# Performance work log

Measured on AMD Instinct MI355X. Metric: run time of the kernel, lower is better.

The kernel has to match this reference:

```python
import jax, jax.numpy as jnp
import numpy as np

EPS = 1e-6
N_HEADS = 16
N_KV_HEADS = 4
HEAD_DIM = 128
DIM = 2048
SEQ = 2048
BATCH = 2


def _make_freqs_cis(seqlen, head_dim, theta=10000.0):
    inv = 1.0 / (theta ** (jnp.arange(0, head_dim, 2, dtype=jnp.float32) / head_dim))  # [hd/2]
    t = jnp.arange(seqlen, dtype=jnp.float32)
    ang = jnp.outer(t, inv)  # [seq, hd/2]
    return jnp.stack([jnp.cos(ang), jnp.sin(ang)], axis=-1)  # [seq, hd/2, 2]


def setup_inputs() -> dict:
    key = jax.random.key(0)
    k1, k2, k3 = jax.random.split(key, 3)
    std = 0.02
    x = jax.random.normal(k1, (BATCH, SEQ, DIM), dtype=jnp.float32)
    freqs_cis = _make_freqs_cis(SEQ, HEAD_DIM)
    norm_w = jnp.ones((DIM,), dtype=jnp.float32)
    wqkv_w = jax.random.normal(k2, ((N_HEADS + 2 * N_KV_HEADS) * HEAD_DIM, DIM), dtype=jnp.float32) * std
    wo_w = jax.random.normal(k3, (DIM, N_HEADS * HEAD_DIM), dtype=jnp.float32) * std
    return {"x": x, "freqs_cis": freqs_cis, "norm_w": norm_w, "wqkv_w": wqkv_w, "wo_w": wo_w}


def _rope(t, cos, sin):
    # t: [b, s, h, hd] viewed as pairs; cos/sin: [s, hd/2]
    b, s, h, hd = t.shape
    tr = t.reshape(b, s, h, hd // 2, 2)
    xr, xi = tr[..., 0], tr[..., 1]
    c = cos[None, :, None, :]
    sn = sin[None, :, None, :]
    out_r = xr * c - xi * sn
    out_i = xr * sn + xi * c
    return jnp.stack([out_r, out_i], axis=-1).reshape(b, s, h, hd)


def reference(x, freqs_cis, norm_w, wqkv_w, wo_w):
    bs, seqlen, dim = x.shape
    n_rep = N_HEADS // N_KV_HEADS
    # RMSNorm
    xn = x * jax.lax.rsqrt(jnp.mean(x * x, axis=-1, keepdims=True) + EPS) * norm_w
    # fused QKV projection
    qkv = jnp.einsum('bsd,ed->bse', xn, wqkv_w)
    q_sz = N_HEADS * HEAD_DIM
    kv_sz = N_KV_HEADS * HEAD_DIM
    xq = qkv[..., :q_sz].reshape(bs, seqlen, N_HEADS, HEAD_DIM)
    xk = qkv[..., q_sz:q_sz + kv_sz].reshape(bs, seqlen, N_KV_HEADS, HEAD_DIM)
    xv = qkv[..., q_sz + kv_sz:].reshape(bs, seqlen, N_KV_HEADS, HEAD_DIM)
    cos, sin = freqs_cis[..., 0], freqs_cis[..., 1]
    xq = _rope(xq, cos, sin)
    xk = _rope(xk, cos, sin)
    # GQA: group q heads so kv broadcast replaces repeat_kv materialization
    q = xq.transpose(0, 2, 1, 3).reshape(bs, N_KV_HEADS, n_rep, seqlen, HEAD_DIM)
    k = xk.transpose(0, 2, 1, 3)  # [b, g, s, d]
    v = xv.transpose(0, 2, 1, 3)
    scale = 1.0 / jnp.sqrt(jnp.float32(HEAD_DIM))
    scores = jnp.einsum('bgrqd,bgkd->bgrqk', q, k) * scale
    causal = jnp.tril(jnp.ones((seqlen, seqlen), dtype=bool))
    scores = jnp.where(causal, scores, jnp.finfo(scores.dtype).min)
    probs = jax.nn.softmax(scores, axis=-1)
    out = jnp.einsum('bgrqk,bgkd->bgrqd', probs, v)
    out = out.reshape(bs, N_HEADS, seqlen, HEAD_DIM).transpose(0, 2, 1, 3).reshape(bs, seqlen, N_HEADS * HEAD_DIM)
    return jnp.einsum('bse,de->bsd', out, wo_w)
```

## Files before the change

### kernel.cpp

```cpp
#include <hip/hip_runtime.h>
#include <cstdint>
#include <cstddef>

typedef __bf16 bhalf;
typedef __bf16 bhalf8 __attribute__((ext_vector_type(8)));
typedef __bf16 bhalf4 __attribute__((ext_vector_type(4)));
typedef float f32x4 __attribute__((ext_vector_type(4)));

#define RMS_EPS 1e-6f
#define N_HEADS 16
#define N_KV 4
#define HD 128
#define DIM 2048
#define SEQ 2048
#define BATCH 2

static __device__ __forceinline__ f32x4 mfma16(bhalf8 a, bhalf8 b, f32x4 c) {
    return __builtin_amdgcn_mfma_f32_16x16x32_bf16(a, b, c, 0, 0, 0);
}

static __device__ __forceinline__ void gload16(const bhalf* g, bhalf* l) {
    __builtin_amdgcn_global_load_lds((const __attribute__((address_space(1))) unsigned int*)g,
                                     (__attribute__((address_space(3))) unsigned int*)l,
                                     16, 0, 0);
}

__global__ __launch_bounds__(256) void cvt_w(const float* __restrict__ a,
                                             const float* __restrict__ b,
                                             bhalf* __restrict__ dst) {
    size_t i = ((size_t)blockIdx.x * 256 + threadIdx.x) * 4;
    const size_t NQ = (size_t)3072 * 2048;
    float4 v = (i < NQ) ? ((const float4*)a)[i >> 2] : ((const float4*)b)[(i - NQ) >> 2];
    bhalf4 o;
    o[0] = (bhalf)v.x; o[1] = (bhalf)v.y; o[2] = (bhalf)v.z; o[3] = (bhalf)v.w;
    *(bhalf4*)(dst + i) = o;
}

__global__ __launch_bounds__(256) void rmsnorm_k(const float* __restrict__ x,
                                                 const float* __restrict__ w,
                                                 bhalf* __restrict__ xn) {
    const int row = blockIdx.x;
    const int tid = threadIdx.x;
    const float4* xr = (const float4*)(x + (size_t)row * DIM);
    float4 v0 = xr[tid * 2], v1 = xr[tid * 2 + 1];
    float ss = v0.x * v0.x + v0.y * v0.y + v0.z * v0.z + v0.w * v0.w
             + v1.x * v1.x + v1.y * v1.y + v1.z * v1.z + v1.w * v1.w;
    #pragma unroll
    for (int off = 32; off; off >>= 1) ss += __shfl_xor(ss, off, 64);
    __shared__ float red[4];
    if ((tid & 63) == 0) red[tid >> 6] = ss;
    __syncthreads();
    float tot = red[0] + red[1] + red[2] + red[3];
    float scale = rsqrtf(tot * (1.0f / DIM) + RMS_EPS);
    const float4* wr = (const float4*)w;
    float4 w0 = wr[tid * 2], w1 = wr[tid * 2 + 1];
    bhalf8 o;
    o[0] = (bhalf)(v0.x * scale * w0.x); o[1] = (bhalf)(v0.y * scale * w0.y);
    o[2] = (bhalf)(v0.z * scale * w0.z); o[3] = (bhalf)(v0.w * scale * w0.w);
    o[4] = (bhalf)(v1.x * scale * w1.x); o[5] = (bhalf)(v1.y * scale * w1.y);
    o[6] = (bhalf)(v1.z * scale * w1.z); o[7] = (bhalf)(v1.w * scale * w1.w);
    *(bhalf8*)(xn + (size_t)row * DIM + tid * 8) = o;
}

__global__ __launch_bounds__(256) void gemm_abt(const bhalf* __restrict__ A,
                                                const bhalf* __restrict__ B,
                                                float* __restrict__ C,
                                                int N, int K) {
    const int tid = threadIdx.x;
    const int wave = tid >> 6, lane = tid & 63;
    const int quad = lane >> 4, r16 = lane & 15;
    const int m0 = blockIdx.y * 128, n0 = blockIdx.x * 128;
    const int wm = (wave >> 1) * 64, wn = (wave & 1) * 64;

    __shared__ __align__(16) bhalf sA[128][32];
    __shared__ __align__(16) bhalf sB[128][32];

    f32x4 acc[4][4];
    #pragma unroll
    for (int i = 0; i < 4; ++i)
        #pragma unroll
        for (int j = 0; j < 4; ++j) acc[i][j] = (f32x4)0.0f;

    const int lrow = lane >> 2;
    const int lcol = (lane & 3) * 8;
    const int arow = 32 * wave + lrow;
    const bhalf* Ap = A + (size_t)(m0 + arow) * K + lcol;
    const bhalf* Bp = B + (size_t)(n0 + arow) * K + lcol;
    const size_t rs16 = (size_t)16 * K;
    bhalf* sAp0 = &sA[32 * wave][0];
    bhalf* sAp1 = &sA[32 * wave + 16][0];
    bhalf* sBp0 = &sB[32 * wave][0];
    bhalf* sBp1 = &sB[32 * wave + 16][0];

    for (int k0 = 0; k0 < K; k0 += 32) {
        __syncthreads();
        gload16(Ap + k0, sAp0);
        gload16(Ap + k0 + rs16, sAp1);
        gload16(Bp + k0, sBp0);
        gload16(Bp + k0 + rs16, sBp1);
        __syncthreads();
        bhalf8 af[4], bfr[4];
        #pragma unroll
        for (int i = 0; i < 4; ++i) af[i]  = *(bhalf8*)&sA[wm + i * 16 + r16][quad * 8];
        #pragma unroll
        for (int j = 0; j < 4; ++j) bfr[j] = *(bhalf8*)&sB[wn + j * 16 + r16][quad * 8];
        #pragma unroll
        for (int i = 0; i < 4; ++i)
            #pragma unroll
            for (int j = 0; j < 4; ++j)
                acc[i][j] = mfma16(af[i], bfr[j], acc[i][j]);
    }

    #pragma unroll
    for (int i = 0; i < 4; ++i) {
        const int rbase = m0 + wm + i * 16 + quad * 4;
        #pragma unroll
        for (int rr = 0; rr < 4; ++rr) {
            float* crow = C + (size_t)(rbase + rr) * N + n0 + wn + r16;
            #pragma unroll
            for (int j = 0; j < 4; ++j) crow[j * 16] = acc[i][j][rr];
        }
    }
}

__global__ __launch_bounds__(256) void rope_k(const float* __restrict__ qkv,
                                              const float* __restrict__ freqs,
                                              bhalf* __restrict__ qb,
                                              bhalf* __restrict__ kb,
                                              bhalf* __restrict__ vt) {
    const int bs = blockIdx.x;
    const int b = bs >> 11, s = bs & 2047;
    const float* row = qkv + (size_t)bs * 3072;
    const int tid = threadIdx.x;

    {
        const int h = tid >> 4, d20 = (tid & 15) * 4;
        const float* rp = row + h * HD + d20 * 2;
        float4 e0 = *(const float4*)rp;
        float4 e1 = *(const float4*)(rp + 4);
        const float* fp = freqs + (size_t)s * 128 + d20 * 2;
        float4 f0 = *(const float4*)fp;
        float4 f1 = *(const float4*)(fp + 4);
        bhalf8 o;
        o[0] = (bhalf)(e0.x * f0.x - e0.y * f0.y); o[1] = (bhalf)(e0.x * f0.y + e0.y * f0.x);
        o[2] = (bhalf)(e0.z * f0.z - e0.w * f0.w); o[3] = (bhalf)(e0.z * f0.w + e0.w * f0.z);
        o[4] = (bhalf)(e1.x * f1.x - e1.y * f1.y); o[5] = (bhalf)(e1.x * f1.y + e1.y * f1.x);
        o[6] = (bhalf)(e1.z * f1.z - e1.w * f1.w); o[7] = (bhalf)(e1.z * f1.w + e1.w * f1.z);
        *(bhalf8*)(qb + ((size_t)(b * N_HEADS + h) * SEQ + s) * HD + d20 * 2) = o;
    }
    if (tid < 64) {
        const int kh = tid >> 4, d20 = (tid & 15) * 4;
        const float* rp = row + 2048 + kh * HD + d20 * 2;
        float4 e0 = *(const float4*)rp;
        float4 e1 = *(const float4*)(rp + 4);
        const float* fp = freqs + (size_t)s * 128 + d20 * 2;
        float4 f0 = *(const float4*)fp;
        float4 f1 = *(const float4*)(fp + 4);
        bhalf8 o;
        o[0] = (bhalf)(e0.x * f0.x - e0.y * f0.y); o[1] = (bhalf)(e0.x * f0.y + e0.y * f0.x);
        o[2] = (bhalf)(e0.z * f0.z - e0.w * f0.w); o[3] = (bhalf)(e0.z * f0.w + e0.w * f0.z);
        o[4] = (bhalf)(e1.x * f1.x - e1.y * f1.y); o[5] = (bhalf)(e1.x * f1.y + e1.y * f1.x);
        o[6] = (bhalf)(e1.z * f1.z - e1.w * f1.w); o[7] = (bhalf)(e1.z * f1.w + e1.w * f1.z);
        *(bhalf8*)(kb + ((size_t)(b * N_KV + kh) * SEQ + s) * HD + d20 * 2) = o;
    }
    for (int e = tid; e < 512; e += 256) {
        const int kh = e >> 7, d = e & 127;
        vt[((size_t)(b * N_KV + kh) * HD + d) * SEQ + s] = (bhalf)row[2560 + e];
    }
}

__global__ __launch_bounds__(256, 2) void attn_k(const bhalf* __restrict__ qb,
                                                 const bhalf* __restrict__ kb,
                                                 const bhalf* __restrict__ vt,
                                                 bhalf* __restrict__ ob) {
    const int tid = threadIdx.x;
    const int wave = tid >> 6, lane = tid & 63;
    const int quad = lane >> 4, r16 = lane & 15;
    const int pair = blockIdx.x & 15;
    const int h = (blockIdx.x >> 4) & 15;
    const int b = blockIdx.x >> 8;
    const int kvh = h >> 2;

    __shared__ __align__(16) bhalf sK[64][136];
    __shared__ __align__(16) bhalf sV[128][72];
    __shared__ __align__(16) bhalf sP[4][16][72];

    const bhalf* Kbase = kb + (size_t)(b * N_KV + kvh) * SEQ * HD;
    const bhalf* Vbase = vt + (size_t)(b * N_KV + kvh) * HD * SEQ;
    const float SCL2 = 0.08838834764831845f * 1.4426950408889634f;

    const int kr = tid >> 4, kc = (tid & 15) * 8;
    const int vr = tid >> 3, vc = (tid & 7) * 8;
    const int gat = (lane & 48);

    for (int phase = 0; phase < 2; ++phase) {
        const int qt = phase ? (31 - pair) : pair;

        const bhalf* qbase = qb + (((size_t)(b * N_HEADS + h) * SEQ) + qt * 64 + wave * 16 + r16) * HD;
        bhalf8 qf[4];
        #pragma unroll
        for (int kk = 0; kk < 4; ++kk) {
            bhalf8 q0 = *(const bhalf8*)(qbase + kk * 32 + quad * 8);
            #pragma unroll
            for (int e = 0; e < 8; ++e) q0[e] = (bhalf)((float)q0[e] * SCL2);
            qf[kk] = q0;
        }

        f32x4 accO[8];
        #pragma unroll
        for (int dt = 0; dt < 8; ++dt) accO[dt] = (f32x4)0.0f;
        float m_i = -1e30f, l_i = 0.0f;

        bhalf8 kreg[4], vreg[4];
        #pragma unroll
        for (int i = 0; i < 4; ++i) {
            kreg[i] = *(const bhalf8*)(Kbase + (size_t)(kr + 16 * i) * HD + kc);
            vreg[i] = *(const bhalf8*)(Vbase + (size_t)(vr + 32 * i) * SEQ + vc);
        }

        for (int kt = 0; kt <= qt; ++kt) {
            __syncthreads();
            #pragma unroll
            for (int i = 0; i < 4; ++i) {
                *(bhalf8*)&sK[kr + 16 * i][kc] = kreg[i];
                *(bhalf8*)&sV[vr + 32 * i][vc] = vreg[i];
            }
            __syncthreads();
            if (kt < qt) {
                const int kn = (kt + 1) * 64;
                #pragma unroll
                for (int i = 0; i < 4; ++i) {
                    kreg[i] = *(const bhalf8*)(Kbase + (size_t)(kn + kr + 16 * i) * HD + kc);
                    vreg[i] = *(const bhalf8*)(Vbase + (size_t)(vr + 32 * i) * SEQ + kn + vc);
                }
            }

            f32x4 accS[4];
            #pragma unroll
            for (int nt = 0; nt < 4; ++nt) accS[nt] = (f32x4)0.0f;
            #pragma unroll
            for (int nt = 0; nt < 4; ++nt)
                #pragma unroll
                for (int kk = 0; kk < 4; ++kk) {
                    bhalf8 kf = *(bhalf8*)&sK[nt * 16 + r16][kk * 32 + quad * 8];
                    accS[nt] = mfma16(kf, qf[kk], accS[nt]);
                }
            if (kt == qt) {
                #pragma unroll
                for (int nt = 0; nt < 4; ++nt)
                    #pragma unroll
                    for (int r = 0; r < 4; ++r)
                        if (nt * 16 + quad * 4 + r > wave * 16 + r16) accS[nt][r] = -1e30f;
            }

            float mx = -1e30f;
            #pragma unroll
            for (int nt = 0; nt < 4; ++nt)
                #pragma unroll
                for (int r = 0; r < 4; ++r) mx = fmaxf(mx, accS[nt][r]);
            mx = fmaxf(mx, __shfl_xor(mx, 16, 64));
            mx = fmaxf(mx, __shfl_xor(mx, 32, 64));
            const float mnew = fmaxf(m_i, mx);
            const float alpha = exp2f(m_i - mnew);
            m_i = mnew;

            float rs = 0.0f;
            #pragma unroll
            for (int nt = 0; nt < 4; ++nt) {
                bhalf4 pk;
                #pragma unroll
                for (int r = 0; r < 4; ++r) {
                    float p = exp2f(accS[nt][r] - mnew);
                    rs += p;
                    pk[r] = (bhalf)p;
                }
                *(bhalf4*)&sP[wave][r16][nt * 16 + quad * 4] = pk;
            }
            rs += __shfl_xor(rs, 16, 64);
            rs += __shfl_xor(rs, 32, 64);
            l_i = l_i * alpha + rs;

            float alphar[4];
            #pragma unroll
            for (int r = 0; r < 4; ++r) alphar[r] = __shfl(alpha, gat | (quad * 4 + r), 64);
            #pragma unroll
            for (int dt = 0; dt < 8; ++dt)
                #pragma unroll
                for (int r = 0; r < 4; ++r) accO[dt][r] *= alphar[r];

            #pragma unroll
            for (int kk2 = 0; kk2 < 2; ++kk2) {
                bhalf8 pf = *(bhalf8*)&sP[wave][r16][kk2 * 32 + quad * 8];
                #pragma unroll
                for (int dt = 0; dt < 8; ++dt) {
                    bhalf8 vf = *(bhalf8*)&sV[dt * 16 + r16][kk2 * 32 + quad * 8];
                    accO[dt] = mfma16(pf, vf, accO[dt]);
                }
            }
        }

        const float linv = 1.0f / l_i;
        float inv[4];
        #pragma unroll
        for (int r = 0; r < 4; ++r) inv[r] = __shfl(linv, gat | (quad * 4 + r), 64);
        const size_t obase = ((size_t)b * SEQ + qt * 64 + wave * 16) * (size_t)(N_HEADS * HD) + h * HD;
        #pragma unroll
        for (int dt = 0; dt < 8; ++dt)
            #pragma unroll
            for (int r = 0; r < 4; ++r)
                ob[obase + (size_t)(quad * 4 + r) * (N_HEADS * HD) + dt * 16 + r16] =
                    (bhalf)(accO[dt][r] * inv[r]);
    }
}

extern "C" void kernel_launch(void* const* d_in, const int* in_sizes, int n_in,
                              void* d_out, int out_size, void* d_ws, size_t ws_size,
                              hipStream_t stream) {
    const float* x      = (const float*)d_in[0];
    const float* freqs  = (const float*)d_in[1];
    const float* norm_w = (const float*)d_in[2];
    const float* wqkv   = (const float*)d_in[3];
    const float* wo     = (const float*)d_in[4];
    float* out = (float*)d_out;

    char* ws = (char*)d_ws;
    bhalf* wqkv_b = (bhalf*)(ws);
    bhalf* wo_b   = (bhalf*)(ws + 12582912);
    bhalf* xn     = (bhalf*)(ws + 20971520);
    float* qkv    = (float*)(ws + 37748736);
    bhalf* qb     = (bhalf*)(ws + 88080384);
    bhalf* kb     = (bhalf*)(ws + 104857600);
    bhalf* vtb    = (bhalf*)(ws + 109051904);
    bhalf* attn   = (bhalf*)(ws + 113246208);

    cvt_w<<<10240, 256, 0, stream>>>(wqkv, wo, wqkv_b);
    rmsnorm_k<<<BATCH * SEQ, 256, 0, stream>>>(x, norm_w, xn);
    gemm_abt<<<dim3(24, 32), 256, 0, stream>>>(xn, wqkv_b, qkv, 3072, 2048);
    rope_k<<<BATCH * SEQ, 256, 0, stream>>>(qkv, freqs, qb, kb, vtb);
    attn_k<<<512, 256, 0, stream>>>(qb, kb, vtb, attn);
    gemm_abt<<<dim3(16, 32), 256, 0, stream>>>(attn, wo_b, out, 2048, 2048);
}
```

Baseline: 341.3 us.

## Switch attention to 32x32 MFMA with 128-row query tiles; emit bf16 QKV

The attention kernel now uses 32x32x16 bf16 MFMA instructions, with each wave owning 32 query rows and each block covering a 128-row query tile. The grid is halved to 256 blocks, launch bounds drop to one block per SM, and waves whose rows lie entirely before a key tile skip it. This is meant to cut LDS fragment reads and cross-lane shuffles per FLOP, at the cost of lower occupancy and coarser causal load balancing. Separately, the QKV GEMM now writes bf16 instead of fp32, halving the intermediate traffic that the rope kernel reads.

```diff
diff --git a/kernel.cpp b/kernel.cpp
--- a/kernel.cpp
+++ b/kernel.cpp
@@ -6,6 +6,7 @@
 typedef __bf16 bhalf8 __attribute__((ext_vector_type(8)));
 typedef __bf16 bhalf4 __attribute__((ext_vector_type(4)));
 typedef float f32x4 __attribute__((ext_vector_type(4)));
+typedef float f32x16 __attribute__((ext_vector_type(16)));
 
 #define RMS_EPS 1e-6f
 #define N_HEADS 16
@@ -17,6 +18,9 @@
 
 static __device__ __forceinline__ f32x4 mfma16(bhalf8 a, bhalf8 b, f32x4 c) {
     return __builtin_amdgcn_mfma_f32_16x16x32_bf16(a, b, c, 0, 0, 0);
+}
+static __device__ __forceinline__ f32x16 mfma32(bhalf8 a, bhalf8 b, f32x16 c) {
+    return __builtin_amdgcn_mfma_f32_32x32x16_bf16(a, b, c, 0, 0, 0);
 }
 
 static __device__ __forceinline__ void gload16(const bhalf* g, bhalf* l) {
@@ -62,9 +66,10 @@
     *(bhalf8*)(xn + (size_t)row * DIM + tid * 8) = o;
 }
 
+template <typename OutT>
 __global__ __launch_bounds__(256) void gemm_abt(const bhalf* __restrict__ A,
                                                 const bhalf* __restrict__ B,
-                                                float* __restrict__ C,
+                                                OutT* __restrict__ C,
                                                 int N, int K) {
     const int tid = threadIdx.x;
     const int wave = tid >> 6, lane = tid & 63;
@@ -116,74 +121,78 @@
         const int rbase = m0 + wm + i * 16 + quad * 4;
         #pragma unroll
         for (int rr = 0; rr < 4; ++rr) {
-            float* crow = C + (size_t)(rbase + rr) * N + n0 + wn + r16;
-            #pragma unroll
-            for (int j = 0; j < 4; ++j) crow[j * 16] = acc[i][j][rr];
+            OutT* crow = C + (size_t)(rbase + rr) * N + n0 + wn + r16;
+            #pragma unroll
+            for (int j = 0; j < 4; ++j) crow[j * 16] = (OutT)acc[i][j][rr];
         }
     }
 }
 
-__global__ __launch_bounds__(256) void rope_k(const float* __restrict__ qkv,
+__global__ __launch_bounds__(256) void rope_k(const bhalf* __restrict__ qkv,
                                               const float* __restrict__ freqs,
                                               bhalf* __restrict__ qb,
                                               bhalf* __restrict__ kb,
                                               bhalf* __restrict__ vt) {
     const int bs = blockIdx.x;
     const int b = bs >> 11, s = bs & 2047;
-    const float* row = qkv + (size_t)bs * 3072;
+    const bhalf* row = qkv + (size_t)bs * 3072;
     const int tid = threadIdx.x;
 
     {
         const int h = tid >> 4, d20 = (tid & 15) * 4;
-        const float* rp = row + h * HD + d20 * 2;
-        float4 e0 = *(const float4*)rp;
-        float4 e1 = *(const float4*)(rp + 4);
+        bhalf8 e = *(const bhalf8*)(row + h * HD + d20 * 2);
         const float* fp = freqs + (size_t)s * 128 + d20 * 2;
         float4 f0 = *(const float4*)fp;
         float4 f1 = *(const float4*)(fp + 4);
         bhalf8 o;
-        o[0] = (bhalf)(e0.x * f0.x - e0.y * f0.y); o[1] = (bhalf)(e0.x * f0.y + e0.y * f0.x);
-        o[2] = (bhalf)(e0.z * f0.z - e0.w * f0.w); o[3] = (bhalf)(e0.z * f0.w + e0.w * f0.z);
-        o[4] = (bhalf)(e1.x * f1.x - e1.y * f1.y); o[5] = (bhalf)(e1.x * f1.y + e1.y * f1.x);
-        o[6] = (bhalf)(e1.z * f1.z - e1.w * f1.w); o[7] = (bhalf)(e1.z * f1.w + e1.w * f1.z);
+        o[0] = (bhalf)((float)e[0] * f0.x - (float)e[1] * f0.y);
+        o[1] = (bhalf)((float)e[0] * f0.y + (float)e[1] * f0.x);
+        o[2] = (bhalf)((float)e[2] * f0.z - (float)e[3] * f0.w);
+        o[3] = (bhalf)((float)e[2] * f0.w + (float)e[3] * f0.z);
+        o[4] = (bhalf)((float)e[4] * f1.x - (float)e[5] * f1.y);
+        o[5] = (bhalf)((float)e[4] * f1.y + (float)e[5] * f1.x);
+        o[6] = (bhalf)((float)e[6] * f1.z - (float)e[7] * f1.w);
+        o[7] = (bhalf)((float)e[6] * f1.w + (float)e[7] * f1.z);
         *(bhalf8*)(qb + ((size_t)(b * N_HEADS + h) * SEQ + s) * HD + d20 * 2) = o;
     }
     if (tid < 64) {
         const int kh = tid >> 4, d20 = (tid & 15) * 4;
-        const float* rp = row + 2048 + kh * HD + d20 * 2;
-        float4 e0 = *(const float4*)rp;
-        float4 e1 = *(const float4*)(rp + 4);
+        bhalf8 e = *(const bhalf8*)(row + 2048 + kh * HD + d20 * 2);
         const float* fp = freqs + (size_t)s * 128 + d20 * 2;
         float4 f0 = *(const float4*)fp;
         float4 f1 = *(const float4*)(fp + 4);
         bhalf8 o;
-        o[0] = (bhalf)(e0.x * f0.x - e0.y * f0.y); o[1] = (bhalf)(e0.x * f0.y + e0.y * f0.x);
-        o[2] = (bhalf)(e0.z * f0.z - e0.w * f0.w); o[3] = (bhalf)(e0.z * f0.w + e0.w * f0.z);
-        o[4] = (bhalf)(e1.x * f1.x - e1.y * f1.y); o[5] = (bhalf)(e1.x * f1.y + e1.y * f1.x);
-        o[6] = (bhalf)(e1.z * f1.z - e1.w * f1.w); o[7] = (bhalf)(e1.z * f1.w + e1.w * f1.z);
+        o[0] = (bhalf)((float)e[0] * f0.x - (float)e[1] * f0.y);
+        o[1] = (bhalf)((float)e[0] * f0.y + (float)e[1] * f0.x);
+        o[2] = (bhalf)((float)e[2] * f0.z - (float)e[3] * f0.w);
+        o[3] = (bhalf)((float)e[2] * f0.w + (float)e[3] * f0.z);
+        o[4] = (bhalf)((float)e[4] * f1.x - (float)e[5] * f1.y);
+        o[5] = (bhalf)((float)e[4] * f1.y + (float)e[5] * f1.x);
+        o[6] = (bhalf)((float)e[6] * f1.z - (float)e[7] * f1.w);
+        o[7] = (bhalf)((float)e[6] * f1.w + (float)e[7] * f1.z);
         *(bhalf8*)(kb + ((size_t)(b * N_KV + kh) * SEQ + s) * HD + d20 * 2) = o;
     }
     for (int e = tid; e < 512; e += 256) {
         const int kh = e >> 7, d = e & 127;
-        vt[((size_t)(b * N_KV + kh) * HD + d) * SEQ + s] = (bhalf)row[2560 + e];
-    }
-}
-
-__global__ __launch_bounds__(256, 2) void attn_k(const bhalf* __restrict__ qb,
+        vt[((size_t)(b * N_KV + kh) * HD + d) * SEQ + s] = row[2560 + e];
+    }
+}
+
+__global__ __launch_bounds__(256, 1) void attn_k(const bhalf* __restrict__ qb,
                                                  const bhalf* __restrict__ kb,
                                                  const bhalf* __restrict__ vt,
                                                  bhalf* __restrict__ ob) {
     const int tid = threadIdx.x;
     const int wave = tid >> 6, lane = tid & 63;
-    const int quad = lane >> 4, r16 = lane & 15;
-    const int pair = blockIdx.x & 15;
-    const int h = (blockIdx.x >> 4) & 15;
-    const int b = blockIdx.x >> 8;
-    const int kvh = h >> 2;
+    const int l31 = lane & 31, h2 = lane >> 5;
+    const int pair = blockIdx.x & 7;
+    const int hh = (blockIdx.x >> 3) & 15;
+    const int b = blockIdx.x >> 7;
+    const int kvh = hh >> 2;
 
     __shared__ __align__(16) bhalf sK[64][136];
     __shared__ __align__(16) bhalf sV[128][72];
-    __shared__ __align__(16) bhalf sP[4][16][72];
+    __shared__ __align__(16) bhalf sP[4][32][72];
 
     const bhalf* Kbase = kb + (size_t)(b * N_KV + kvh) * SEQ * HD;
     const bhalf* Vbase = vt + (size_t)(b * N_KV + kvh) * HD * SEQ;
@@ -191,24 +200,25 @@
 
     const int kr = tid >> 4, kc = (tid & 15) * 8;
     const int vr = tid >> 3, vc = (tid & 7) * 8;
-    const int gat = (lane & 48);
 
     for (int phase = 0; phase < 2; ++phase) {
-        const int qt = phase ? (31 - pair) : pair;
-
-        const bhalf* qbase = qb + (((size_t)(b * N_HEADS + h) * SEQ) + qt * 64 + wave * 16 + r16) * HD;
-        bhalf8 qf[4];
-        #pragma unroll
-        for (int kk = 0; kk < 4; ++kk) {
-            bhalf8 q0 = *(const bhalf8*)(qbase + kk * 32 + quad * 8);
+        const int qt = phase ? (15 - pair) : pair;
+        const int ktmax = 2 * qt + 1;
+        const int qrow = qt * 128 + wave * 32 + l31;
+
+        const bhalf* qbase = qb + (((size_t)(b * N_HEADS + hh) * SEQ) + qrow) * HD;
+        bhalf8 qf[8];
+        #pragma unroll
+        for (int kk = 0; kk < 8; ++kk) {
+            bhalf8 q0 = *(const bhalf8*)(qbase + kk * 16 + h2 * 8);
             #pragma unroll
             for (int e = 0; e < 8; ++e) q0[e] = (bhalf)((float)q0[e] * SCL2);
             qf[kk] = q0;
         }
 
-        f32x4 accO[8];
-        #pragma unroll
-        for (int dt = 0; dt < 8; ++dt) accO[dt] = (f32x4)0.0f;
+        f32x16 accO[4];
+        #pragma unroll
+        for (int dt = 0; dt < 4; ++dt) accO[dt] = (f32x16)0.0f;
         float m_i = -1e30f, l_i = 0.0f;
 
         bhalf8 kreg[4], vreg[4];
@@ -218,7 +228,7 @@
             vreg[i] = *(const bhalf8*)(Vbase + (size_t)(vr + 32 * i) * SEQ + vc);
         }
 
-        for (int kt = 0; kt <= qt; ++kt) {
+        for (int kt = 0; kt <= ktmax; ++kt) {
             __syncthreads();
             #pragma unroll
             for (int i = 0; i < 4; ++i) {
@@ -226,7 +236,7 @@
                 *(bhalf8*)&sV[vr + 32 * i][vc] = vreg[i];
             }
             __syncthreads();
-            if (kt < qt) {
+            if (kt < ktmax) {
                 const int kn = (kt + 1) * 64;
                 #pragma unroll
                 for (int i = 0; i < 4; ++i) {
@@ -235,30 +245,32 @@
                 }
             }
 
-            f32x4 accS[4];
-            #pragma unroll
-            for (int nt = 0; nt < 4; ++nt) accS[nt] = (f32x4)0.0f;
-            #pragma unroll
-            for (int nt = 0; nt < 4; ++nt)
-                #pragma unroll
-                for (int kk = 0; kk < 4; ++kk) {
-                    bhalf8 kf = *(bhalf8*)&sK[nt * 16 + r16][kk * 32 + quad * 8];
-                    accS[nt] = mfma16(kf, qf[kk], accS[nt]);
-                }
-            if (kt == qt) {
-                #pragma unroll
-                for (int nt = 0; nt < 4; ++nt)
+            if (qt * 128 + wave * 32 + 31 < kt * 64) continue;
+
+            f32x16 accS[2];
+            accS[0] = (f32x16)0.0f; accS[1] = (f32x16)0.0f;
+            #pragma unroll
+            for (int kk = 0; kk < 8; ++kk) {
+                bhalf8 kf0 = *(bhalf8*)&sK[l31][kk * 16 + h2 * 8];
+                bhalf8 kf1 = *(bhalf8*)&sK[32 + l31][kk * 16 + h2 * 8];
+                accS[0] = mfma32(kf0, qf[kk], accS[0]);
+                accS[1] = mfma32(kf1, qf[kk], accS[1]);
+            }
+            if (kt * 64 + 63 > qt * 128 + wave * 32) {
+                #pragma unroll
+                for (int nt = 0; nt < 2; ++nt)
                     #pragma unroll
-                    for (int r = 0; r < 4; ++r)
-                        if (nt * 16 + quad * 4 + r > wave * 16 + r16) accS[nt][r] = -1e30f;
+                    for (int r = 0; r < 16; ++r) {
+                        const int key = kt * 64 + nt * 32 + (r & 3) + 8 * (r >> 2) + 4 * h2;
+                        if (key > qrow) accS[nt][r] = -1e30f;
+                    }
             }
 
             float mx = -1e30f;
             #pragma unroll
-            for (int nt = 0; nt < 4; ++nt)
-                #pragma unroll
-                for (int r = 0; r < 4; ++r) mx = fmaxf(mx, accS[nt][r]);
-            mx = fmaxf(mx, __shfl_xor(mx, 16, 64));
+            for (int nt = 0; nt < 2; ++nt)
+                #pragma unroll
+                for (int r = 0; r < 16; ++r) mx = fmaxf(mx, accS[nt][r]);
             mx = fmaxf(mx, __shfl_xor(mx, 32, 64));
             const float mnew = fmaxf(m_i, mx);
             const float alpha = exp2f(m_i - mnew);
@@ -266,50 +278,48 @@
 
             float rs = 0.0f;
             #pragma unroll
-            for (int nt = 0; nt < 4; ++nt) {
-                bhalf4 pk;
-                #pragma unroll
-                for (int r = 0; r < 4; ++r) {
-                    float p = exp2f(accS[nt][r] - mnew);
-                    rs += p;
-                    pk[r] = (bhalf)p;
+            for (int nt = 0; nt < 2; ++nt)
+                #pragma unroll
+                for (int c = 0; c < 4; ++c) {
+                    bhalf4 pk;
+                    #pragma unroll
+                    for (int r = 0; r < 4; ++r) {
+                        float p = exp2f(accS[nt][c * 4 + r] - mnew);
+                        rs += p;
+                        pk[r] = (bhalf)p;
+                    }
+                    *(bhalf4*)&sP[wave][l31][nt * 32 + c * 8 + h2 * 4] = pk;
                 }
-                *(bhalf4*)&sP[wave][r16][nt * 16 + quad * 4] = pk;
-            }
-            rs += __shfl_xor(rs, 16, 64);
             rs += __shfl_xor(rs, 32, 64);
             l_i = l_i * alpha + rs;
 
-            float alphar[4];
-            #pragma unroll
-            for (int r = 0; r < 4; ++r) alphar[r] = __shfl(alpha, gat | (quad * 4 + r), 64);
-            #pragma unroll
-            for (int dt = 0; dt < 8; ++dt)
-                #pragma unroll
-                for (int r = 0; r < 4; ++r) accO[dt][r] *= alphar[r];
-
-            #pragma unroll
-            for (int kk2 = 0; kk2 < 2; ++kk2) {
-                bhalf8 pf = *(bhalf8*)&sP[wave][r16][kk2 * 32 + quad * 8];
-                #pragma unroll
-                for (int dt = 0; dt < 8; ++dt) {
-                    bhalf8 vf = *(bhalf8*)&sV[dt * 16 + r16][kk2 * 32 + quad * 8];
-                    accO[dt] = mfma16(pf, vf, accO[dt]);
+            #pragma unroll
+            for (int dt = 0; dt < 4; ++dt)
+                #pragma unroll
+                for (int r = 0; r < 16; ++r) accO[dt][r] *= alpha;
+
+            #pragma unroll
+            for (int kk2 = 0; kk2 < 4; ++kk2) {
+                bhalf8 pf = *(bhalf8*)&sP[wave][l31][kk2 * 16 + h2 * 8];
+                #pragma unroll
+                for (int dt = 0; dt < 4; ++dt) {
+                    bhalf8 vf = *(bhalf8*)&sV[dt * 32 + l31][kk2 * 16 + h2 * 8];
+                    accO[dt] = mfma32(vf, pf, accO[dt]);
                 }
             }
         }
 
-        const float linv = 1.0f / l_i;
-        float inv[4];
-        #pragma unroll
-        for (int r = 0; r < 4; ++r) inv[r] = __shfl(linv, gat | (quad * 4 + r), 64);
-        const size_t obase = ((size_t)b * SEQ + qt * 64 + wave * 16) * (size_t)(N_HEADS * HD) + h * HD;
-        #pragma unroll
-        for (int dt = 0; dt < 8; ++dt)
-            #pragma unroll
-            for (int r = 0; r < 4; ++r)
-                ob[obase + (size_t)(quad * 4 + r) * (N_HEADS * HD) + dt * 16 + r16] =
-                    (bhalf)(accO[dt][r] * inv[r]);
+        const float inv = 1.0f / l_i;
+        bhalf* obase = ob + ((size_t)b * SEQ + qrow) * (size_t)(N_HEADS * HD) + hh * HD;
+        #pragma unroll
+        for (int dt = 0; dt < 4; ++dt)
+            #pragma unroll
+            for (int c = 0; c < 4; ++c) {
+                bhalf4 o4;
+                #pragma unroll
+                for (int r = 0; r < 4; ++r) o4[r] = (bhalf)(accO[dt][c * 4 + r] * inv);
+                *(bhalf4*)(obase + dt * 32 + c * 8 + h2 * 4) = o4;
+            }
     }
 }
 
@@ -327,7 +337,7 @@
     bhalf* wqkv_b = (bhalf*)(ws);
     bhalf* wo_b   = (bhalf*)(ws + 12582912);
     bhalf* xn     = (bhalf*)(ws + 20971520);
-    float* qkv    = (float*)(ws + 37748736);
+    bhalf* qkv    = (bhalf*)(ws + 37748736);
     bhalf* qb     = (bhalf*)(ws + 88080384);
     bhalf* kb     = (bhalf*)(ws + 104857600);
     bhalf* vtb    = (bhalf*)(ws + 109051904);
@@ -335,8 +345,8 @@
 
     cvt_w<<<10240, 256, 0, stream>>>(wqkv, wo, wqkv_b);
     rmsnorm_k<<<BATCH * SEQ, 256, 0, stream>>>(x, norm_w, xn);
-    gemm_abt<<<dim3(24, 32), 256, 0, stream>>>(xn, wqkv_b, qkv, 3072, 2048);
+    gemm_abt<bhalf><<<dim3(24, 32), 256, 0, stream>>>(xn, wqkv_b, qkv, 3072, 2048);
     rope_k<<<BATCH * SEQ, 256, 0, stream>>>(qkv, freqs, qb, kb, vtb);
-    attn_k<<<512, 256, 0, stream>>>(qb, kb, vtb, attn);
-    gemm_abt<<<dim3(16, 32), 256, 0, stream>>>(attn, wo_b, out, 2048, 2048);
-}
+    attn_k<<<256, 256, 0, stream>>>(qb, kb, vtb, attn);
+    gemm_abt<float><<<dim3(16, 32), 256, 0, stream>>>(attn, wo_b, out, 2048, 2048);
+}
```

Result: no change. 336.0 us (-1.6%).
